# Kernel optimization log

Measured on AMD Instinct MI355X. Metric: run time of the kernel, lower is better.

The kernel has to match this reference:

```python
import jax, jax.numpy as jnp
import numpy as np

N = 2048
FEAT = 64 + 512 + 4096 + 32768 + 192 + 216  # 37848 actual concat width

# 54 neighbor offsets: dx,dy,dz in {-1,0,1}, dt in {-1,1}
_OFFSETS = np.array([[dx, dy, dz, dt]
                     for dx in (-1, 0, 1)
                     for dy in (-1, 0, 1)
                     for dz in (-1, 0, 1)
                     for dt in (-1, 1)], dtype=np.int32)


def setup_inputs() -> dict:
    key = jax.random.key(0)
    ks = jax.random.split(key, 12)
    pos = jax.random.uniform(ks[0], (N, 3), dtype=jnp.float32)
    dir = jax.random.normal(ks[1], (N, 3), dtype=jnp.float32)
    t = jax.random.uniform(ks[2], (N,), dtype=jnp.float32)
    table0 = jax.random.normal(ks[3], (128, 128, 128, 64), dtype=jnp.float32)
    table1 = jax.random.normal(ks[4], (64, 64, 64, 512), dtype=jnp.float32)
    table2 = jax.random.normal(ks[5], (32, 32, 32, 4096), dtype=jnp.float32)
    table3 = jax.random.normal(ks[6], (16, 16, 16, 32768), dtype=jnp.float32)
    ts_table1 = jax.random.normal(ks[7], (16, 16, 16, 64, 64), dtype=jnp.float32)
    ts_table2 = jax.random.normal(ks[8], (128, 128, 128, 128, 4), dtype=jnp.float32)
    W_mlp = jax.random.normal(ks[9], (128, FEAT), dtype=jnp.float32) * 0.01
    W_proj = jax.random.normal(ks[10], (4, 132), dtype=jnp.float32) * 0.1
    b_proj = jnp.zeros((4,), dtype=jnp.float32)
    return dict(pos=pos, dir=dir, t=t, table0=table0, table1=table1,
                table2=table2, table3=table3, ts_table1=ts_table1,
                ts_table2=ts_table2, W_mlp=W_mlp, W_proj=W_proj, b_proj=b_proj)


def _gather3(table, idx):
    return table[idx[:, 0], idx[:, 1], idx[:, 2]]


def reference(pos, dir, t, table0, table1, table2, table3,
              ts_table1, ts_table2, W_mlp, W_proj, b_proj):
    idx0 = (pos * 127).astype(jnp.int32)
    idx1 = (pos * 63).astype(jnp.int32)
    idx2 = (pos * 31).astype(jnp.int32)
    idx3 = (pos * 15).astype(jnp.int32)
    t_idx = (t * 127).astype(jnp.int32)            # [N]
    idx4 = jnp.concatenate([idx3, t_idx[:, None]], axis=-1)  # [N,4]

    f0 = _gather3(table0, idx0)   # [N,64]
    f1 = _gather3(table1, idx1)   # [N,512]
    f2 = _gather3(table2, idx2)   # [N,4096]
    f3 = _gather3(table3, idx3)   # [N,32768]

    # time table: spatial idx3, time index wrapped mod 64 for delta in {-1,0,1}
    def ts1(delta):
        ti = jnp.mod(t_idx + delta, 64)
        return ts_table1[idx3[:, 0], idx3[:, 1], idx3[:, 2], ti]  # [N,64]
    time_feats = jnp.concatenate([ts1(-1), ts1(0), ts1(1)], axis=-1)  # [N,192]

    # 54 modulo-wrapped 4D neighbor lookups, vectorized
    dims4 = jnp.array([128, 128, 128, 128], dtype=jnp.int32)
    nb = jnp.mod(idx4[:, None, :] + jnp.asarray(_OFFSETS)[None, :, :], dims4)  # [N,54,4]
    nb_feats = ts_table2[nb[..., 0], nb[..., 1], nb[..., 2], nb[..., 3]]       # [N,54,4]
    nb_feats = nb_feats.reshape(nb_feats.shape[0], -1)                          # [N,216]

    all_feats = jnp.concatenate([f0, f1, f2, f3, time_feats, nb_feats], axis=-1)  # [N,37848]
    all_feats = jax.nn.relu(all_feats)  # F.relu then model_sequence ReLU (idempotent)
    downsized = all_feats @ W_mlp.T     # [N,128]

    final = jnp.concatenate([downsized, dir, t[:, None]], axis=-1)  # [N,132]
    return final @ W_proj.T + b_proj     # [N,4]
```

## Files before the change

kernel.cpp:

```cpp
#include <hip/hip_runtime.h>


#define N_PTS 2048
#define KP_TOTAL 37888
#define K_ORIG 37848
#define KS3 8
#define CPB 8
#define FOLD_BLOCKS 592

__global__ __launch_bounds__(256) void setup_kernel(
    const float* __restrict__ Wm, const float* __restrict__ Wproj,
    float* __restrict__ Wf, const float* __restrict__ pos,
    int* __restrict__ list, int* __restrict__ count) {

    const int b = blockIdx.x;
    const int tid = threadIdx.x;

    if (b < FOLD_BLOCKS) {
        __shared__ float red[4][64][4];
        const int kpl = tid & 63;
        const int jq  = tid >> 6;
        const int kp  = b * 64 + kpl;
        int k; bool valid = true;
        if (kp < 576)        k = kp;
        else if (kp < 768)   k = 37440 + (kp - 576);
        else if (kp < 984)   k = 37632 + (kp - 768);
        else if (kp < 1024)  { k = 0; valid = false; }
        else if (kp < 5120)  k = 576 + (kp - 1024);
        else                 k = 4672 + (kp - 5120);
        float a0 = 0.f, a1 = 0.f, a2 = 0.f, a3 = 0.f;
        if (valid) {
            const float* wk = Wm + k;
            const int j0 = jq * 32;
            #pragma unroll
            for (int jj = 0; jj < 32; ++jj) {
                const int j = j0 + jj;
                const float w = wk[(size_t)j * K_ORIG];
                a0 = fmaf(Wproj[0 * 132 + j], w, a0);
                a1 = fmaf(Wproj[1 * 132 + j], w, a1);
                a2 = fmaf(Wproj[2 * 132 + j], w, a2);
                a3 = fmaf(Wproj[3 * 132 + j], w, a3);
            }
        }
        red[jq][kpl][0] = a0; red[jq][kpl][1] = a1;
        red[jq][kpl][2] = a2; red[jq][kpl][3] = a3;
        __syncthreads();
        const int rkpl = tid >> 2, rch = tid & 3;
        const float s = red[0][rkpl][rch] + red[1][rkpl][rch]
                      + red[2][rkpl][rch] + red[3][rkpl][rch];
        Wf[(size_t)rch * KP_TOTAL + b * 64 + rkpl] = s;
        return;
    }

    __shared__ int flags[4096];
    __shared__ int cnt;
    for (int i = tid; i < 4096; i += 256) flags[i] = 0;
    if (tid == 0) cnt = 0;
    __syncthreads();
    #pragma unroll
    for (int q = 0; q < 8; ++q) {
        const int n = q * 256 + tid;
        const float px = pos[3 * n], py = pos[3 * n + 1], pz = pos[3 * n + 2];
        const int i3 = (int)(px * 15.f), j3 = (int)(py * 15.f), k3 = (int)(pz * 15.f);
        const int cell = (i3 * 16 + j3) * 16 + k3;
        if (atomicExch(&flags[cell], 1) == 0) {
            const int p = atomicAdd(&cnt, 1);
            list[p] = cell;
        }
    }
    __syncthreads();
    if (tid == 0) count[0] = cnt;
}

__global__ __launch_bounds__(256) void celldot_kernel(
    const float* __restrict__ table3, const float* __restrict__ Wf,
    const int* __restrict__ list, const int* __restrict__ count,
    float* __restrict__ cellpart) {

    const int cnt = count[0];
    const int yb = blockIdx.y;
    if (yb * CPB >= cnt) return;
    const int ks = blockIdx.x;
    const int tid = threadIdx.x;

    int cell[CPB]; const float* rowp[CPB];
    #pragma unroll
    for (int j = 0; j < CPB; ++j) {
        const int idx = yb * CPB + j;
        const int safe = (idx < cnt) ? idx : (cnt - 1);
        cell[j] = list[safe];
        rowp[j] = table3 + (size_t)cell[j] * 32768 + ks * 4096;
    }

    const int qoff = 5120 + ks * 4096;
    const float* wf0 = Wf + (size_t)0 * KP_TOTAL + qoff;
    const float* wf1 = Wf + (size_t)1 * KP_TOTAL + qoff;
    const float* wf2 = Wf + (size_t)2 * KP_TOTAL + qoff;
    const float* wf3 = Wf + (size_t)3 * KP_TOTAL + qoff;

    float accv[CPB][4];
    #pragma unroll
    for (int j = 0; j < CPB; ++j)
        #pragma unroll
        for (int c = 0; c < 4; ++c) accv[j][c] = 0.f;

    #pragma unroll
    for (int kk = 0; kk < 4; ++kk) {
        const int off = kk * 1024 + tid * 4;
        const float4 w0 = *(const float4*)(wf0 + off);
        const float4 w1 = *(const float4*)(wf1 + off);
        const float4 w2 = *(const float4*)(wf2 + off);
        const float4 w3 = *(const float4*)(wf3 + off);
        #pragma unroll
        for (int j = 0; j < CPB; ++j) {
            float4 r = *(const float4*)(rowp[j] + off);
            r.x = fmaxf(r.x, 0.f); r.y = fmaxf(r.y, 0.f);
            r.z = fmaxf(r.z, 0.f); r.w = fmaxf(r.w, 0.f);
            accv[j][0] = fmaf(r.x, w0.x, fmaf(r.y, w0.y, fmaf(r.z, w0.z, fmaf(r.w, w0.w, accv[j][0]))));
            accv[j][1] = fmaf(r.x, w1.x, fmaf(r.y, w1.y, fmaf(r.z, w1.z, fmaf(r.w, w1.w, accv[j][1]))));
            accv[j][2] = fmaf(r.x, w2.x, fmaf(r.y, w2.y, fmaf(r.z, w2.z, fmaf(r.w, w2.w, accv[j][2]))));
            accv[j][3] = fmaf(r.x, w3.x, fmaf(r.y, w3.y, fmaf(r.z, w3.z, fmaf(r.w, w3.w, accv[j][3]))));
        }
    }

    #pragma unroll
    for (int s = 1; s < 64; s <<= 1)
        #pragma unroll
        for (int j = 0; j < CPB; ++j)
            #pragma unroll
            for (int c = 0; c < 4; ++c)
                accv[j][c] += __shfl_xor(accv[j][c], s);

    __shared__ float red[4][CPB * 4];
    const int wv = tid >> 6, ln = tid & 63;
    if (ln == 0)
        #pragma unroll
        for (int j = 0; j < CPB; ++j)
            #pragma unroll
            for (int c = 0; c < 4; ++c)
                red[wv][j * 4 + c] = accv[j][c];
    __syncthreads();
    if (tid < CPB * 4) {
        const float s = red[0][tid] + red[1][tid] + red[2][tid] + red[3][tid];
        const int j = tid >> 2, c = tid & 3;
        if (yb * CPB + j < cnt)
            cellpart[((size_t)ks * 4096 + cell[j]) * 4 + c] = s;
    }
}

__global__ __launch_bounds__(256) void point_kernel(
    const float* __restrict__ pos, const float* __restrict__ dir,
    const float* __restrict__ t,
    const float* __restrict__ table0, const float* __restrict__ table1,
    const float* __restrict__ table2,
    const float* __restrict__ ts1, const float* __restrict__ ts2,
    const float* __restrict__ Wf, const float* __restrict__ cellpart,
    const float* __restrict__ Wproj, const float* __restrict__ bproj,
    float* __restrict__ out) {

    const int n = blockIdx.x;
    const int tid = threadIdx.x;

    const float px = pos[3 * n], py = pos[3 * n + 1], pz = pos[3 * n + 2];
    const float tv = t[n];
    const int i0 = (int)(px * 127.f), j0 = (int)(py * 127.f), k0 = (int)(pz * 127.f);
    const int i1 = (int)(px * 63.f),  j1 = (int)(py * 63.f),  k1 = (int)(pz * 63.f);
    const int i2 = (int)(px * 31.f),  j2 = (int)(py * 31.f),  k2 = (int)(pz * 31.f);
    const int i3 = (int)(px * 15.f),  j3 = (int)(py * 15.f),  k3 = (int)(pz * 15.f);
    const int ti = (int)(tv * 127.f);
    const int cell = (i3 * 16 + j3) * 16 + k3;

    const float* f0p = table0 + (size_t)((i0 * 128 + j0) * 128 + k0) * 64;
    const float* f1p = table1 + (size_t)((i1 * 64 + j1) * 64 + k1) * 512;
    const float* f2p = table2 + (size_t)((i2 * 32 + j2) * 32 + k2) * 4096;
    const float* t1p = ts1 + (size_t)cell * 4096;

    float a0 = 0.f, a1 = 0.f, a2 = 0.f, a3 = 0.f;

    #pragma unroll
    for (int s5 = 0; s5 < 5; ++s5) {
        const int slot = s5 * 256 + tid;
        float4 f;
        bool have = true;
        if (slot >= 256) {
            f = *(const float4*)(f2p + (slot - 256) * 4);
        } else if (slot < 16) {
            f = *(const float4*)(f0p + slot * 4);
        } else if (slot < 144) {
            f = *(const float4*)(f1p + (slot - 16) * 4);
        } else if (slot < 192) {
            const int s2 = slot - 144;
            const int d = s2 >> 4;
            const int e4 = (s2 & 15) * 4;
            const int tw = (ti + d - 1 + 64) & 63;
            f = *(const float4*)(t1p + tw * 64 + e4);
        } else if (slot < 246) {
            const int o = slot - 192;
            const int dt_ = (o & 1) ? 1 : -1;
            const int rest = o >> 1;
            const int dz_ = rest % 3 - 1;
            const int dy_ = (rest / 3) % 3 - 1;
            const int dx_ = rest / 9 - 1;
            const int x = (i3 + dx_ + 128) & 127;
            const int y = (j3 + dy_ + 128) & 127;
            const int z = (k3 + dz_ + 128) & 127;
            const int w = (ti + dt_ + 128) & 127;
            f = *(const float4*)(ts2 + ((size_t)((x * 128 + y) * 128 + z) * 128 + w) * 4);
        } else {
            have = false;
        }
        if (have) {
            f.x = fmaxf(f.x, 0.f); f.y = fmaxf(f.y, 0.f);
            f.z = fmaxf(f.z, 0.f); f.w = fmaxf(f.w, 0.f);
            const int kp = slot * 4;
            const float4 w0 = *(const float4*)(Wf + (size_t)0 * KP_TOTAL + kp);
            const float4 w1 = *(const float4*)(Wf + (size_t)1 * KP_TOTAL + kp);
            const float4 w2 = *(const float4*)(Wf + (size_t)2 * KP_TOTAL + kp);
            const float4 w3 = *(const float4*)(Wf + (size_t)3 * KP_TOTAL + kp);
            a0 = fmaf(f.x, w0.x, fmaf(f.y, w0.y, fmaf(f.z, w0.z, fmaf(f.w, w0.w, a0))));
            a1 = fmaf(f.x, w1.x, fmaf(f.y, w1.y, fmaf(f.z, w1.z, fmaf(f.w, w1.w, a1))));
            a2 = fmaf(f.x, w2.x, fmaf(f.y, w2.y, fmaf(f.z, w2.z, fmaf(f.w, w2.w, a2))));
            a3 = fmaf(f.x, w3.x, fmaf(f.y, w3.y, fmaf(f.z, w3.z, fmaf(f.w, w3.w, a3))));
        }
    }

    #pragma unroll
    for (int s = 1; s < 64; s <<= 1) {
        a0 += __shfl_xor(a0, s);
        a1 += __shfl_xor(a1, s);
        a2 += __shfl_xor(a2, s);
        a3 += __shfl_xor(a3, s);
    }
    __shared__ float red[4][4];
    const int wv = tid >> 6, ln = tid & 63;
    if (ln == 0) { red[wv][0] = a0; red[wv][1] = a1; red[wv][2] = a2; red[wv][3] = a3; }
    __syncthreads();
    if (tid < 4) {
        float s = red[0][tid] + red[1][tid] + red[2][tid] + red[3][tid];
        #pragma unroll
        for (int ks = 0; ks < KS3; ++ks)
            s += cellpart[((size_t)ks * 4096 + cell) * 4 + tid];
        s += dir[3 * n]     * Wproj[tid * 132 + 128];
        s += dir[3 * n + 1] * Wproj[tid * 132 + 129];
        s += dir[3 * n + 2] * Wproj[tid * 132 + 130];
        s += tv             * Wproj[tid * 132 + 131];
        s += bproj[tid];
        out[n * 4 + tid] = s;
    }
}

extern "C" void kernel_launch(void* const* d_in, const int* in_sizes, int n_in,
                              void* d_out, int out_size, void* d_ws, size_t ws_size,
                              hipStream_t stream) {
    const float* pos    = (const float*)d_in[0];
    const float* dir    = (const float*)d_in[1];
    const float* t      = (const float*)d_in[2];
    const float* table0 = (const float*)d_in[3];
    const float* table1 = (const float*)d_in[4];
    const float* table2 = (const float*)d_in[5];
    const float* table3 = (const float*)d_in[6];
    const float* ts1    = (const float*)d_in[7];
    const float* ts2    = (const float*)d_in[8];
    const float* Wm     = (const float*)d_in[9];
    const float* Wproj  = (const float*)d_in[10];
    const float* bproj  = (const float*)d_in[11];
    float* out = (float*)d_out;

    char* ws = (char*)d_ws;
    float* Wf       = (float*)(ws);
    float* cellpart = (float*)(ws + 606208);
    int*   list     = (int*)(ws + 1130496);
    int*   count    = (int*)(ws + 1146880);

    hipLaunchKernelGGL(setup_kernel, dim3(FOLD_BLOCKS + 1), dim3(256), 0, stream,
                       Wm, Wproj, Wf, pos, list, count);
    hipLaunchKernelGGL(celldot_kernel, dim3(KS3, 256), dim3(256), 0, stream,
                       table3, Wf, list, count, cellpart);
    hipLaunchKernelGGL(point_kernel, dim3(N_PTS), dim3(256), 0, stream,
                       pos, dir, t, table0, table1, table2, ts1, ts2,
                       Wf, cellpart, Wproj, bproj, out);
}
```

Baseline: 63.99 us.

## Merge cell-dot and point kernels into one launch with a small final combine

Fuses the per-cell table3 dot-product blocks and the per-point gather blocks into a single grid, with block index deciding the role. This lets the two independent workloads overlap on the GPU instead of running back to back, which removes the tail of the cell kernel and one dependency boundary. A small final kernel then adds the cell partials to the per-point partials. The cost is an extra launch, an extra partial buffer round trip, and larger shared-memory and register use per block because both roles live in one kernel.

```diff
diff --git a/kernel.cpp b/kernel.cpp
--- a/kernel.cpp
+++ b/kernel.cpp
@@ -6,6 +6,7 @@
 #define K_ORIG 37848
 #define KS3 8
 #define CPB 8
+#define NB_CD 2048
 #define FOLD_BLOCKS 592
 
 __global__ __launch_bounds__(256) void setup_kernel(
@@ -72,94 +73,94 @@
     if (tid == 0) count[0] = cnt;
 }
 
-__global__ __launch_bounds__(256) void celldot_kernel(
+__global__ __launch_bounds__(256) void mega_kernel(
     const float* __restrict__ table3, const float* __restrict__ Wf,
     const int* __restrict__ list, const int* __restrict__ count,
-    float* __restrict__ cellpart) {
-
-    const int cnt = count[0];
-    const int yb = blockIdx.y;
-    if (yb * CPB >= cnt) return;
-    const int ks = blockIdx.x;
-    const int tid = threadIdx.x;
-
-    int cell[CPB]; const float* rowp[CPB];
-    #pragma unroll
-    for (int j = 0; j < CPB; ++j) {
-        const int idx = yb * CPB + j;
-        const int safe = (idx < cnt) ? idx : (cnt - 1);
-        cell[j] = list[safe];
-        rowp[j] = table3 + (size_t)cell[j] * 32768 + ks * 4096;
-    }
-
-    const int qoff = 5120 + ks * 4096;
-    const float* wf0 = Wf + (size_t)0 * KP_TOTAL + qoff;
-    const float* wf1 = Wf + (size_t)1 * KP_TOTAL + qoff;
-    const float* wf2 = Wf + (size_t)2 * KP_TOTAL + qoff;
-    const float* wf3 = Wf + (size_t)3 * KP_TOTAL + qoff;
-
-    float accv[CPB][4];
-    #pragma unroll
-    for (int j = 0; j < CPB; ++j)
-        #pragma unroll
-        for (int c = 0; c < 4; ++c) accv[j][c] = 0.f;
-
-    #pragma unroll
-    for (int kk = 0; kk < 4; ++kk) {
-        const int off = kk * 1024 + tid * 4;
-        const float4 w0 = *(const float4*)(wf0 + off);
-        const float4 w1 = *(const float4*)(wf1 + off);
-        const float4 w2 = *(const float4*)(wf2 + off);
-        const float4 w3 = *(const float4*)(wf3 + off);
-        #pragma unroll
-        for (int j = 0; j < CPB; ++j) {
-            float4 r = *(const float4*)(rowp[j] + off);
-            r.x = fmaxf(r.x, 0.f); r.y = fmaxf(r.y, 0.f);
-            r.z = fmaxf(r.z, 0.f); r.w = fmaxf(r.w, 0.f);
-            accv[j][0] = fmaf(r.x, w0.x, fmaf(r.y, w0.y, fmaf(r.z, w0.z, fmaf(r.w, w0.w, accv[j][0]))));
-            accv[j][1] = fmaf(r.x, w1.x, fmaf(r.y, w1.y, fmaf(r.z, w1.z, fmaf(r.w, w1.w, accv[j][1]))));
-            accv[j][2] = fmaf(r.x, w2.x, fmaf(r.y, w2.y, fmaf(r.z, w2.z, fmaf(r.w, w2.w, accv[j][2]))));
-            accv[j][3] = fmaf(r.x, w3.x, fmaf(r.y, w3.y, fmaf(r.z, w3.z, fmaf(r.w, w3.w, accv[j][3]))));
-        }
-    }
-
-    #pragma unroll
-    for (int s = 1; s < 64; s <<= 1)
-        #pragma unroll
-        for (int j = 0; j < CPB; ++j)
-            #pragma unroll
-            for (int c = 0; c < 4; ++c)
-                accv[j][c] += __shfl_xor(accv[j][c], s);
-
-    __shared__ float red[4][CPB * 4];
-    const int wv = tid >> 6, ln = tid & 63;
-    if (ln == 0)
-        #pragma unroll
-        for (int j = 0; j < CPB; ++j)
-            #pragma unroll
-            for (int c = 0; c < 4; ++c)
-                red[wv][j * 4 + c] = accv[j][c];
-    __syncthreads();
-    if (tid < CPB * 4) {
-        const float s = red[0][tid] + red[1][tid] + red[2][tid] + red[3][tid];
-        const int j = tid >> 2, c = tid & 3;
-        if (yb * CPB + j < cnt)
-            cellpart[((size_t)ks * 4096 + cell[j]) * 4 + c] = s;
-    }
-}
-
-__global__ __launch_bounds__(256) void point_kernel(
+    float* __restrict__ cellpart,
     const float* __restrict__ pos, const float* __restrict__ dir,
     const float* __restrict__ t,
     const float* __restrict__ table0, const float* __restrict__ table1,
     const float* __restrict__ table2,
     const float* __restrict__ ts1, const float* __restrict__ ts2,
-    const float* __restrict__ Wf, const float* __restrict__ cellpart,
     const float* __restrict__ Wproj, const float* __restrict__ bproj,
-    float* __restrict__ out) {
-
-    const int n = blockIdx.x;
+    float* __restrict__ pointpart) {
+
+    const int b = blockIdx.x;
     const int tid = threadIdx.x;
+
+    if (b < NB_CD) {
+        const int cnt = count[0];
+        const int ks = b & 7;
+        const int yb = b >> 3;
+        if (yb * CPB >= cnt) return;
+
+        int cell[CPB]; const float* rowp[CPB];
+        #pragma unroll
+        for (int j = 0; j < CPB; ++j) {
+            const int idx = yb * CPB + j;
+            const int safe = (idx < cnt) ? idx : (cnt - 1);
+            cell[j] = list[safe];
+            rowp[j] = table3 + (size_t)cell[j] * 32768 + ks * 4096;
+        }
+
+        const int qoff = 5120 + ks * 4096;
+        const float* wf0 = Wf + (size_t)0 * KP_TOTAL + qoff;
+        const float* wf1 = Wf + (size_t)1 * KP_TOTAL + qoff;
+        const float* wf2 = Wf + (size_t)2 * KP_TOTAL + qoff;
+        const float* wf3 = Wf + (size_t)3 * KP_TOTAL + qoff;
+
+        float accv[CPB][4];
+        #pragma unroll
+        for (int j = 0; j < CPB; ++j)
+            #pragma unroll
+            for (int c = 0; c < 4; ++c) accv[j][c] = 0.f;
+
+        #pragma unroll
+        for (int kk = 0; kk < 4; ++kk) {
+            const int off = kk * 1024 + tid * 4;
+            const float4 w0 = *(const float4*)(wf0 + off);
+            const float4 w1 = *(const float4*)(wf1 + off);
+            const float4 w2 = *(const float4*)(wf2 + off);
+            const float4 w3 = *(const float4*)(wf3 + off);
+            #pragma unroll
+            for (int j = 0; j < CPB; ++j) {
+                float4 r = *(const float4*)(rowp[j] + off);
+                r.x = fmaxf(r.x, 0.f); r.y = fmaxf(r.y, 0.f);
+                r.z = fmaxf(r.z, 0.f); r.w = fmaxf(r.w, 0.f);
+                accv[j][0] = fmaf(r.x, w0.x, fmaf(r.y, w0.y, fmaf(r.z, w0.z, fmaf(r.w, w0.w, accv[j][0]))));
+                accv[j][1] = fmaf(r.x, w1.x, fmaf(r.y, w1.y, fmaf(r.z, w1.z, fmaf(r.w, w1.w, accv[j][1]))));
+                accv[j][2] = fmaf(r.x, w2.x, fmaf(r.y, w2.y, fmaf(r.z, w2.z, fmaf(r.w, w2.w, accv[j][2]))));
+                accv[j][3] = fmaf(r.x, w3.x, fmaf(r.y, w3.y, fmaf(r.z, w3.z, fmaf(r.w, w3.w, accv[j][3]))));
+            }
+        }
+
+        #pragma unroll
+        for (int s = 1; s < 64; s <<= 1)
+            #pragma unroll
+            for (int j = 0; j < CPB; ++j)
+                #pragma unroll
+                for (int c = 0; c < 4; ++c)
+                    accv[j][c] += __shfl_xor(accv[j][c], s);
+
+        __shared__ float redc[4][CPB * 4];
+        const int wv = tid >> 6, ln = tid & 63;
+        if (ln == 0)
+            #pragma unroll
+            for (int j = 0; j < CPB; ++j)
+                #pragma unroll
+                for (int c = 0; c < 4; ++c)
+                    redc[wv][j * 4 + c] = accv[j][c];
+        __syncthreads();
+        if (tid < CPB * 4) {
+            const float s = redc[0][tid] + redc[1][tid] + redc[2][tid] + redc[3][tid];
+            const int j = tid >> 2, c = tid & 3;
+            if (yb * CPB + j < cnt)
+                cellpart[((size_t)ks * 4096 + cell[j]) * 4 + c] = s;
+        }
+        return;
+    }
+
+    const int n = b - NB_CD;
 
     const float px = pos[3 * n], py = pos[3 * n + 1], pz = pos[3 * n + 2];
     const float tv = t[n];
@@ -231,22 +232,35 @@
         a2 += __shfl_xor(a2, s);
         a3 += __shfl_xor(a3, s);
     }
-    __shared__ float red[4][4];
+    __shared__ float redp[4][4];
     const int wv = tid >> 6, ln = tid & 63;
-    if (ln == 0) { red[wv][0] = a0; red[wv][1] = a1; red[wv][2] = a2; red[wv][3] = a3; }
+    if (ln == 0) { redp[wv][0] = a0; redp[wv][1] = a1; redp[wv][2] = a2; redp[wv][3] = a3; }
     __syncthreads();
     if (tid < 4) {
-        float s = red[0][tid] + red[1][tid] + red[2][tid] + red[3][tid];
-        #pragma unroll
-        for (int ks = 0; ks < KS3; ++ks)
-            s += cellpart[((size_t)ks * 4096 + cell) * 4 + tid];
+        float s = redp[0][tid] + redp[1][tid] + redp[2][tid] + redp[3][tid];
         s += dir[3 * n]     * Wproj[tid * 132 + 128];
         s += dir[3 * n + 1] * Wproj[tid * 132 + 129];
         s += dir[3 * n + 2] * Wproj[tid * 132 + 130];
         s += tv             * Wproj[tid * 132 + 131];
         s += bproj[tid];
-        out[n * 4 + tid] = s;
-    }
+        pointpart[n * 4 + tid] = s;
+    }
+}
+
+__global__ __launch_bounds__(256) void final_kernel(
+    const float* __restrict__ pointpart, const float* __restrict__ cellpart,
+    const float* __restrict__ pos, float* __restrict__ out) {
+    const int tid = threadIdx.x;
+    const int n = blockIdx.x * 64 + (tid >> 2);
+    const int c = tid & 3;
+    const float px = pos[3 * n], py = pos[3 * n + 1], pz = pos[3 * n + 2];
+    const int i3 = (int)(px * 15.f), j3 = (int)(py * 15.f), k3 = (int)(pz * 15.f);
+    const int cell = (i3 * 16 + j3) * 16 + k3;
+    float s = pointpart[n * 4 + c];
+    #pragma unroll
+    for (int ks = 0; ks < KS3; ++ks)
+        s += cellpart[((size_t)ks * 4096 + cell) * 4 + c];
+    out[n * 4 + c] = s;
 }
 
 extern "C" void kernel_launch(void* const* d_in, const int* in_sizes, int n_in,
@@ -267,16 +281,18 @@
     float* out = (float*)d_out;
 
     char* ws = (char*)d_ws;
-    float* Wf       = (float*)(ws);
-    float* cellpart = (float*)(ws + 606208);
-    int*   list     = (int*)(ws + 1130496);
-    int*   count    = (int*)(ws + 1146880);
+    float* Wf        = (float*)(ws);
+    float* cellpart  = (float*)(ws + 606208);
+    int*   list      = (int*)(ws + 1130496);
+    int*   count     = (int*)(ws + 1146880);
+    float* pointpart = (float*)(ws + 1146944);
 
     hipLaunchKernelGGL(setup_kernel, dim3(FOLD_BLOCKS + 1), dim3(256), 0, stream,
                        Wm, Wproj, Wf, pos, list, count);
-    hipLaunchKernelGGL(celldot_kernel, dim3(KS3, 256), dim3(256), 0, stream,
-                       table3, Wf, list, count, cellpart);
-    hipLaunchKernelGGL(point_kernel, dim3(N_PTS), dim3(256), 0, stream,
+    hipLaunchKernelGGL(mega_kernel, dim3(NB_CD + N_PTS), dim3(256), 0, stream,
+                       table3, Wf, list, count, cellpart,
                        pos, dir, t, table0, table1, table2, ts1, ts2,
-                       Wf, cellpart, Wproj, bproj, out);
-}
+                       Wproj, bproj, pointpart);
+    hipLaunchKernelGGL(final_kernel, dim3(32), dim3(256), 0, stream,
+                       pointpart, cellpart, pos, out);
+}
```

Measured after the change: 61.09 us (median of 2 runs). 4.5% less time.
